# Performance work log

Measured on AMD Instinct MI355X. Metric: run time of the kernel, lower is better.

The kernel has to match this reference:

```python
import jax, jax.numpy as jnp
import numpy as np

DIM = 512
HEADS = 8
DIM_HEAD = 64
INNER = HEADS * DIM_HEAD  # 512
EPS = 1e-6


def setup_inputs() -> dict:
    key = jax.random.key(0)
    ks = jax.random.split(key, 6)
    B, N = 8, 2048
    x = jax.random.normal(ks[0], (B, N, DIM), dtype=jnp.float32)
    # nn.Linear stores weight as [out, in]; we keep that layout and transpose in matmul.
    w_qkv = jax.random.normal(ks[1], (3 * INNER, DIM), dtype=jnp.float32) * (1.0 / np.sqrt(DIM))
    w_proj = jax.random.normal(ks[2], (DIM, INNER), dtype=jnp.float32) * (1.0 / np.sqrt(INNER))
    b_proj = jax.random.normal(ks[3], (DIM,), dtype=jnp.float32) * 0.01
    ln_gamma = jnp.ones((DIM,), dtype=jnp.float32)
    ln_beta = jnp.zeros((DIM,), dtype=jnp.float32)
    return {"x": x, "w_qkv": w_qkv, "w_proj": w_proj, "b_proj": b_proj,
            "ln_gamma": ln_gamma, "ln_beta": ln_beta}


def reference(x, w_qkv, w_proj, b_proj, ln_gamma, ln_beta):
    B, N, D = x.shape
    H, Dh = HEADS, DIM_HEAD
    # LayerNorm (eps=1e-6)
    mu = jnp.mean(x, axis=-1, keepdims=True)
    var = jnp.mean(jnp.square(x - mu), axis=-1, keepdims=True)
    xn = (x - mu) * jax.lax.rsqrt(var + EPS) * ln_gamma + ln_beta
    # QKV projection (no bias)
    qkv = xn @ w_qkv.T  # [B, N, 3*INNER]
    q, k, v = jnp.split(qkv, 3, axis=-1)
    # [B, N, H, Dh] -> [B, H, N, Dh]
    q = q.reshape(B, N, H, Dh).transpose(0, 2, 1, 3)
    k = k.reshape(B, N, H, Dh).transpose(0, 2, 1, 3)
    v = v.reshape(B, N, H, Dh).transpose(0, 2, 1, 3)
    scale = Dh ** (-0.5)
    attn = jnp.einsum('bhnd,bhmd->bhnm', q, k) * scale  # [B, H, N, N]
    attn = jax.nn.softmax(attn, axis=-1)
    out = jnp.einsum('bhnm,bhmd->bhnd', attn, v)  # [B, H, N, Dh]
    out = out.transpose(0, 2, 1, 3).reshape(B, N, H * Dh)
    out = out @ w_proj.T + b_proj
    return out
```

## Files before the change

### kernel.cpp

```cpp
#include <hip/hip_runtime.h>

typedef unsigned short u16;
typedef __bf16 bf16x8 __attribute__((ext_vector_type(8)));
typedef float f32x4 __attribute__((ext_vector_type(4)));

#define DIMD 512
#define SEQN 2048
#define NB   8
#define NH   8
#define DH   64
#define BHN  (NB*NH)
#define MROWS (NB*SEQN)
#define QSCALE 0.18033688f

__device__ __forceinline__ u16 f2bf(float f) {
  union { float f; unsigned u; } x; x.f = f;
  unsigned r = x.u + 0x7fffu + ((x.u >> 16) & 1u);
  return (u16)(r >> 16);
}
__device__ __forceinline__ u16 f2bf_fast(float f) {
  union { float f; unsigned u; } x; x.f = f;
  return (u16)((x.u + 0x8000u) >> 16);
}

__device__ __forceinline__ void gll16(const u16* g, u16* lbase) {
#if __has_builtin(__builtin_amdgcn_global_load_lds)
  __builtin_amdgcn_global_load_lds(
      (const __attribute__((address_space(1))) unsigned int*)g,
      (__attribute__((address_space(3))) unsigned int*)lbase, 16, 0, 0);
#else
  *(uint4*)((u16*)lbase + (threadIdx.x & 63) * 8) = *(const uint4*)g;
#endif
}

__global__ __launch_bounds__(256) void wcvt2(
    const float* __restrict__ wa, const float* __restrict__ wb,
    u16* __restrict__ oa, u16* __restrict__ ob, int na, int nb) {
  int i = (blockIdx.x * 256 + threadIdx.x) * 8;
  const float* src; u16* dst; int idx;
  if (i < na) { src = wa; dst = oa; idx = i; }
  else { idx = i - na; if (idx >= nb) return; src = wb; dst = ob; }
  float4 f0 = *(const float4*)(src + idx);
  float4 f1 = *(const float4*)(src + idx + 4);
  union { uint4 v; u16 s[8]; } u;
  u.s[0] = f2bf(f0.x); u.s[1] = f2bf(f0.y); u.s[2] = f2bf(f0.z); u.s[3] = f2bf(f0.w);
  u.s[4] = f2bf(f1.x); u.s[5] = f2bf(f1.y); u.s[6] = f2bf(f1.z); u.s[7] = f2bf(f1.w);
  *(uint4*)(dst + idx) = u.v;
}

__global__ __launch_bounds__(256) void ln_kernel(
    const float* __restrict__ x, const float* __restrict__ gamma,
    const float* __restrict__ beta, u16* __restrict__ xn) {
  int row = blockIdx.x * 4 + (threadIdx.x >> 6);
  int lane = threadIdx.x & 63;
  const float* xr = x + (size_t)row * DIMD;
  float f[8], g[8], b[8];
  *(float4*)&f[0] = *(const float4*)(xr + lane * 8);
  *(float4*)&f[4] = *(const float4*)(xr + lane * 8 + 4);
  *(float4*)&g[0] = *(const float4*)(gamma + lane * 8);
  *(float4*)&g[4] = *(const float4*)(gamma + lane * 8 + 4);
  *(float4*)&b[0] = *(const float4*)(beta + lane * 8);
  *(float4*)&b[4] = *(const float4*)(beta + lane * 8 + 4);
  float sum = 0.f, sq = 0.f;
#pragma unroll
  for (int i = 0; i < 8; ++i) { sum += f[i]; sq += f[i] * f[i]; }
#pragma unroll
  for (int off = 1; off < 64; off <<= 1) {
    sum += __shfl_xor(sum, off, 64);
    sq  += __shfl_xor(sq, off, 64);
  }
  float mean = sum * (1.0f / DIMD);
  float var = sq * (1.0f / DIMD) - mean * mean;
  float rstd = rsqrtf(var + 1e-6f);
  union { uint4 v; u16 s[8]; } uo;
#pragma unroll
  for (int i = 0; i < 8; ++i)
    uo.s[i] = f2bf((f[i] - mean) * rstd * g[i] + b[i]);
  *(uint4*)(xn + (size_t)row * DIMD + lane * 8) = uo.v;
}

__global__ __launch_bounds__(256) void qkv_gemm(
    const u16* __restrict__ A, const u16* __restrict__ Bm,
    u16* __restrict__ qo, u16* __restrict__ ko, u16* __restrict__ vto) {
  __shared__ __align__(16) u16 la[128 * 64];
  __shared__ __align__(16) u16 lb[128 * 64];
  const int K = DIMD;
  int tid = threadIdx.x;
  int bm = blockIdx.x, bn = blockIdx.y;
  int wid = tid >> 6, lane = tid & 63, lm = lane & 15, quad = lane >> 4;
  int wm = wid >> 1, wn = wid & 1;
  int lsw = lm & 7;
  f32x4 acc[4][4] = {};
  const u16* Ab = A + (size_t)(bm * 128) * K;
  const u16* Bb = Bm + (size_t)(bn * 128) * K;
  int cb_row = lane >> 3, cb_sub = lane & 7;
  int xsrc = (cb_sub ^ cb_row) * 8;
  for (int k0 = 0; k0 < K; k0 += 64) {
    __syncthreads();
#pragma unroll
    for (int r = 0; r < 4; ++r) {
      int seg = wid * 4 + r;
      int row = seg * 8 + cb_row;
      size_t goff = (size_t)row * K + k0 + xsrc;
      gll16(Ab + goff, &la[seg * 512]);
      gll16(Bb + goff, &lb[seg * 512]);
    }
    __syncthreads();
#pragma unroll
    for (int h = 0; h < 2; ++h) {
      bf16x8 af[4], bfr[4];
#pragma unroll
      for (int i = 0; i < 4; ++i)
        af[i] = *(const bf16x8*)&la[(wm * 64 + i * 16 + lm) * 64 + (((h * 4 + quad) ^ lsw) * 8)];
#pragma unroll
      for (int j = 0; j < 4; ++j)
        bfr[j] = *(const bf16x8*)&lb[(wn * 64 + j * 16 + lm) * 64 + (((h * 4 + quad) ^ lsw) * 8)];
#pragma unroll
      for (int i = 0; i < 4; ++i)
#pragma unroll
        for (int j = 0; j < 4; ++j)
          acc[i][j] = __builtin_amdgcn_mfma_f32_16x16x32_bf16(af[i], bfr[j], acc[i][j], 0, 0, 0);
    }
  }
  int part = bn >> 2;
  if (part == 2) {
#pragma unroll
    for (int i = 0; i < 4; ++i)
#pragma unroll
      for (int j = 0; j < 4; ++j) {
        int col = bn * 128 + wn * 64 + j * 16 + lm;
        int rem = col & 511, h = rem >> 6, d = rem & 63;
        int rg = bm * 128 + wm * 64 + i * 16 + quad * 4;
        int b = rg >> 11, nn = rg & 2047;
        union { unsigned long long ll; u16 s4[4]; } pk;
#pragma unroll
        for (int r = 0; r < 4; ++r) pk.s4[r] = f2bf(acc[i][j][r]);
        *(unsigned long long*)&vto[((size_t)(b * NH + h) * DH + d) * SEQN + nn] = pk.ll;
      }
  } else {
    u16* dst = part ? ko : qo;
    float sc = part ? 1.0f : QSCALE;
#pragma unroll
    for (int i = 0; i < 4; ++i)
#pragma unroll
      for (int j = 0; j < 4; ++j) {
        int col = bn * 128 + wn * 64 + j * 16 + lm;
        int rem = col & 511, h = rem >> 6, d = rem & 63;
#pragma unroll
        for (int r = 0; r < 4; ++r) {
          int rg = bm * 128 + wm * 64 + i * 16 + quad * 4 + r;
          int b = rg >> 11, nn = rg & 2047;
          dst[((size_t)(b * NH + h) * SEQN + nn) * DH + d] = f2bf(acc[i][j][r] * sc);
        }
      }
  }
}

__global__ __launch_bounds__(512, 4) void attn_kernel(
    const u16* __restrict__ q, const u16* __restrict__ k,
    const u16* __restrict__ vt, u16* __restrict__ att) {
  __shared__ __align__(16) u16 kt[2][64 * 64];
  __shared__ __align__(16) u16 vtt[2][64 * 64];
  __shared__ __align__(16) u16 plds[8 * 16 * 64];
  int bh = blockIdx.x;
  int wid = threadIdx.x >> 6, lane = threadIdx.x & 63;
  int lm = lane & 15, quad = lane >> 4;
  int qrow0 = blockIdx.y * 256 + wid * 32;
  const u16* qb = q + (size_t)bh * SEQN * DH;
  const u16* kb = k + (size_t)bh * SEQN * DH;
  const u16* vb = vt + (size_t)bh * DH * SEQN;
  u16* pw = plds + wid * (16 * 64);

  int cb_row = lane >> 3, cb_sub = lane & 7;
  int xstage = (cb_sub ^ cb_row) * 8;
  int xsw = quad ^ (lm & 7);
  int lsw = lm & 7;

  bf16x8 ones;
#pragma unroll
  for (int i = 0; i < 8; ++i) ones[i] = (__bf16)1.0f;

  bf16x8 qf[2][2];
#pragma unroll
  for (int g = 0; g < 2; ++g)
#pragma unroll
    for (int c = 0; c < 2; ++c)
      qf[g][c] = *(const bf16x8*)(qb + (size_t)(qrow0 + g * 16 + lm) * DH + c * 32 + quad * 8);

  f32x4 Ot[2][4] = {};
  f32x4 lacc[2] = {};

  auto stage = [&](int bsel, int j0) {
    if (wid < 4) {
#pragma unroll
      for (int i = 0; i < 2; ++i) {
        int seg = wid * 2 + i;
        int row = seg * 8 + cb_row;
        gll16(kb + (size_t)(j0 + row) * DH + xstage, &kt[bsel][seg * 512]);
      }
    } else {
#pragma unroll
      for (int i = 0; i < 2; ++i) {
        int seg = (wid - 4) * 2 + i;
        int row = seg * 8 + cb_row;
        gll16(vb + (size_t)row * SEQN + j0 + xstage, &vtt[bsel][seg * 512]);
      }
    }
  };

  stage(0, 0);
  for (int t = 0; t < SEQN / 64; ++t) {
    int bsel = t & 1;
    __syncthreads();
    if (t + 1 < SEQN / 64) stage(bsel ^ 1, (t + 1) * 64);

    bf16x8 kf[4][2];
#pragma unroll
    for (int js = 0; js < 4; ++js) {
      int row = js * 16 + lm;
      kf[js][0] = *(const bf16x8*)&kt[bsel][row * 64 + xsw * 8];
      kf[js][1] = *(const bf16x8*)&kt[bsel][row * 64 + (xsw ^ 4) * 8];
    }
    bf16x8 pa[2][2];
#pragma unroll
    for (int g = 0; g < 2; ++g) {
#pragma unroll
      for (int js = 0; js < 4; ++js) {
        f32x4 z = {0.f, 0.f, 0.f, 0.f};
        z = __builtin_amdgcn_mfma_f32_16x16x32_bf16(kf[js][0], qf[g][0], z, 0, 0, 0);
        z = __builtin_amdgcn_mfma_f32_16x16x32_bf16(kf[js][1], qf[g][1], z, 0, 0, 0);
        union { unsigned long long ll; u16 s4[4]; } pk;
#pragma unroll
        for (int r = 0; r < 4; ++r)
          pk.s4[r] = f2bf_fast(__builtin_amdgcn_exp2f(z[r]));
        int wc = (js * 2 + (quad >> 1)) ^ lsw;
        *(unsigned long long*)&pw[lm * 64 + wc * 8 + (quad & 1) * 4] = pk.ll;
      }
      pa[g][0] = *(const bf16x8*)&pw[lm * 64 + (quad ^ lsw) * 8];
      pa[g][1] = *(const bf16x8*)&pw[lm * 64 + ((4 + quad) ^ lsw) * 8];
      lacc[g] = __builtin_amdgcn_mfma_f32_16x16x32_bf16(ones, pa[g][0], lacc[g], 0, 0, 0);
      lacc[g] = __builtin_amdgcn_mfma_f32_16x16x32_bf16(ones, pa[g][1], lacc[g], 0, 0, 0);
    }
#pragma unroll
    for (int db = 0; db < 4; ++db) {
      int row = db * 16 + lm;
      bf16x8 va0 = *(const bf16x8*)&vtt[bsel][row * 64 + xsw * 8];
      bf16x8 va1 = *(const bf16x8*)&vtt[bsel][row * 64 + (xsw ^ 4) * 8];
      Ot[0][db] = __builtin_amdgcn_mfma_f32_16x16x32_bf16(va0, pa[0][0], Ot[0][db], 0, 0, 0);
      Ot[0][db] = __builtin_amdgcn_mfma_f32_16x16x32_bf16(va1, pa[0][1], Ot[0][db], 0, 0, 0);
      Ot[1][db] = __builtin_amdgcn_mfma_f32_16x16x32_bf16(va0, pa[1][0], Ot[1][db], 0, 0, 0);
      Ot[1][db] = __builtin_amdgcn_mfma_f32_16x16x32_bf16(va1, pa[1][1], Ot[1][db], 0, 0, 0);
    }
  }
  int b = bh >> 3, h = bh & 7;
#pragma unroll
  for (int g = 0; g < 2; ++g) {
    float inv = 1.0f / lacc[g][0];
    size_t rowoff = ((size_t)(b * SEQN + qrow0 + g * 16 + lm)) * DIMD + h * DH;
#pragma unroll
    for (int db = 0; db < 4; ++db) {
      union { unsigned long long ll; u16 s4[4]; } ok;
#pragma unroll
      for (int r = 0; r < 4; ++r) ok.s4[r] = f2bf(Ot[g][db][r] * inv);
      *(unsigned long long*)&att[rowoff + db * 16 + quad * 4] = ok.ll;
    }
  }
}

__global__ __launch_bounds__(256) void proj_gemm(
    const u16* __restrict__ A, const u16* __restrict__ Bm,
    const float* __restrict__ bias, float* __restrict__ C) {
  __shared__ __align__(16) u16 la[128 * 64];
  __shared__ __align__(16) u16 lb[128 * 64];
  const int K = DIMD, N = DIMD;
  int tid = threadIdx.x;
  int bm = blockIdx.x, bn = blockIdx.y;
  int wid = tid >> 6, lane = tid & 63, lm = lane & 15, quad = lane >> 4;
  int wm = wid >> 1, wn = wid & 1;
  int lsw = lm & 7;
  f32x4 acc[4][4] = {};
  const u16* Ab = A + (size_t)(bm * 128) * K;
  const u16* Bb = Bm + (size_t)(bn * 128) * K;
  int cb_row = lane >> 3, cb_sub = lane & 7;
  int xsrc = (cb_sub ^ cb_row) * 8;
  for (int k0 = 0; k0 < K; k0 += 64) {
    __syncthreads();
#pragma unroll
    for (int r = 0; r < 4; ++r) {
      int seg = wid * 4 + r;
      int row = seg * 8 + cb_row;
      size_t goff = (size_t)row * K + k0 + xsrc;
      gll16(Ab + goff, &la[seg * 512]);
      gll16(Bb + goff, &lb[seg * 512]);
    }
    __syncthreads();
#pragma unroll
    for (int h = 0; h < 2; ++h) {
      bf16x8 af[4], bfr[4];
#pragma unroll
      for (int i = 0; i < 4; ++i)
        af[i] = *(const bf16x8*)&la[(wm * 64 + i * 16 + lm) * 64 + (((h * 4 + quad) ^ lsw) * 8)];
#pragma unroll
      for (int j = 0; j < 4; ++j)
        bfr[j] = *(const bf16x8*)&lb[(wn * 64 + j * 16 + lm) * 64 + (((h * 4 + quad) ^ lsw) * 8)];
#pragma unroll
      for (int i = 0; i < 4; ++i)
#pragma unroll
        for (int j = 0; j < 4; ++j)
          acc[i][j] = __builtin_amdgcn_mfma_f32_16x16x32_bf16(af[i], bfr[j], acc[i][j], 0, 0, 0);
    }
  }
#pragma unroll
  for (int i = 0; i < 4; ++i)
#pragma unroll
    for (int j = 0; j < 4; ++j) {
      int col = bn * 128 + wn * 64 + j * 16 + lm;
      float bv = bias[col];
#pragma unroll
      for (int r = 0; r < 4; ++r) {
        int rg = bm * 128 + wm * 64 + i * 16 + quad * 4 + r;
        C[(size_t)rg * N + col] = acc[i][j][r] + bv;
      }
    }
}

extern "C" void kernel_launch(void* const* d_in, const int* in_sizes, int n_in,
                              void* d_out, int out_size, void* d_ws, size_t ws_size,
                              hipStream_t stream) {
  const float* x      = (const float*)d_in[0];
  const float* w_qkv  = (const float*)d_in[1];
  const float* w_proj = (const float*)d_in[2];
  const float* b_proj = (const float*)d_in[3];
  const float* gamma  = (const float*)d_in[4];
  const float* beta   = (const float*)d_in[5];
  float* out = (float*)d_out;

  const size_t SZ = (size_t)MROWS * DIMD;
  u16* xn  = (u16*)d_ws;
  u16* q   = xn + SZ;
  u16* kk  = q + SZ;
  u16* vt  = kk + SZ;
  u16* wqb = vt + SZ;
  u16* wpb = wqb + (size_t)3 * DIMD * DIMD;
  u16* att = xn;

  const int NQKV = 3 * DIMD * DIMD;
  const int NPRJ = DIMD * DIMD;
  wcvt2<<<dim3((NQKV + NPRJ) / 2048), dim3(256), 0, stream>>>(
      w_qkv, w_proj, wqb, wpb, NQKV, NPRJ);
  ln_kernel<<<dim3(MROWS / 4), dim3(256), 0, stream>>>(x, gamma, beta, xn);
  qkv_gemm<<<dim3(MROWS / 128, (3 * DIMD) / 128), dim3(256), 0, stream>>>(
      xn, wqb, q, kk, vt);
  attn_kernel<<<dim3(BHN, SEQN / 256), dim3(512), 0, stream>>>(q, kk, vt, att);
  proj_gemm<<<dim3(MROWS / 128, DIMD / 128), dim3(256), 0, stream>>>(
      att, wpb, b_proj, out);
}
```

Measured before the change: 220.5 us.

## Swap MFMA operands for vectorized epilogue stores; add setprio and native bf16 converts

The Q/K and projection GEMMs now swap the MFMA A/B operands, so each lane holds four consecutive columns of one row. This lets the epilogues write 8-byte bf16 packs and float4 outputs with a vectorized bias load, replacing the earlier scattered scalar stores. The attention kernel wraps its MFMA groups in s_setprio, uses native __bf16 casts instead of manual bit rounding, and uses a hardware reciprocal for the final normalisation. The bf16 cast changes rounding in the exp path and rcp is approximate, so the numerics shift slightly.

Measured after the change: 217.8 us. No clear change (-1.2%).

```diff
diff --git a/kernel.cpp b/kernel.cpp
--- a/kernel.cpp
+++ b/kernel.cpp
@@ -17,10 +17,6 @@
   union { float f; unsigned u; } x; x.f = f;
   unsigned r = x.u + 0x7fffu + ((x.u >> 16) & 1u);
   return (u16)(r >> 16);
-}
-__device__ __forceinline__ u16 f2bf_fast(float f) {
-  union { float f; unsigned u; } x; x.f = f;
-  return (u16)((x.u + 0x8000u) >> 16);
 }
 
 __device__ __forceinline__ void gll16(const u16* g, u16* lbase) {
@@ -90,6 +86,7 @@
   int wid = tid >> 6, lane = tid & 63, lm = lane & 15, quad = lane >> 4;
   int wm = wid >> 1, wn = wid & 1;
   int lsw = lm & 7;
+  int part = bn >> 2;
   f32x4 acc[4][4] = {};
   const u16* Ab = A + (size_t)(bm * 128) * K;
   const u16* Bb = Bm + (size_t)(bn * 128) * K;
@@ -115,14 +112,21 @@
 #pragma unroll
       for (int j = 0; j < 4; ++j)
         bfr[j] = *(const bf16x8*)&lb[(wn * 64 + j * 16 + lm) * 64 + (((h * 4 + quad) ^ lsw) * 8)];
-#pragma unroll
-      for (int i = 0; i < 4; ++i)
-#pragma unroll
-        for (int j = 0; j < 4; ++j)
-          acc[i][j] = __builtin_amdgcn_mfma_f32_16x16x32_bf16(af[i], bfr[j], acc[i][j], 0, 0, 0);
-    }
-  }
-  int part = bn >> 2;
+      if (part == 2) {
+#pragma unroll
+        for (int i = 0; i < 4; ++i)
+#pragma unroll
+          for (int j = 0; j < 4; ++j)
+            acc[i][j] = __builtin_amdgcn_mfma_f32_16x16x32_bf16(af[i], bfr[j], acc[i][j], 0, 0, 0);
+      } else {
+#pragma unroll
+        for (int i = 0; i < 4; ++i)
+#pragma unroll
+          for (int j = 0; j < 4; ++j)
+            acc[i][j] = __builtin_amdgcn_mfma_f32_16x16x32_bf16(bfr[j], af[i], acc[i][j], 0, 0, 0);
+      }
+    }
+  }
   if (part == 2) {
 #pragma unroll
     for (int i = 0; i < 4; ++i)
@@ -144,14 +148,14 @@
     for (int i = 0; i < 4; ++i)
 #pragma unroll
       for (int j = 0; j < 4; ++j) {
-        int col = bn * 128 + wn * 64 + j * 16 + lm;
-        int rem = col & 511, h = rem >> 6, d = rem & 63;
-#pragma unroll
-        for (int r = 0; r < 4; ++r) {
-          int rg = bm * 128 + wm * 64 + i * 16 + quad * 4 + r;
-          int b = rg >> 11, nn = rg & 2047;
-          dst[((size_t)(b * NH + h) * SEQN + nn) * DH + d] = f2bf(acc[i][j][r] * sc);
-        }
+        int rg = bm * 128 + wm * 64 + i * 16 + lm;
+        int b = rg >> 11, nn = rg & 2047;
+        int col = bn * 128 + wn * 64 + j * 16 + quad * 4;
+        int rem = col & 511, hh = rem >> 6, d = rem & 63;
+        union { unsigned long long ll; __bf16 h4[4]; } pk;
+#pragma unroll
+        for (int r = 0; r < 4; ++r) pk.h4[r] = (__bf16)(acc[i][j][r] * sc);
+        *(unsigned long long*)&dst[((size_t)(b * NH + hh) * SEQN + nn) * DH + d] = pk.ll;
       }
   }
 }
@@ -227,41 +231,47 @@
 #pragma unroll
       for (int js = 0; js < 4; ++js) {
         f32x4 z = {0.f, 0.f, 0.f, 0.f};
+        __builtin_amdgcn_s_setprio(1);
         z = __builtin_amdgcn_mfma_f32_16x16x32_bf16(kf[js][0], qf[g][0], z, 0, 0, 0);
         z = __builtin_amdgcn_mfma_f32_16x16x32_bf16(kf[js][1], qf[g][1], z, 0, 0, 0);
-        union { unsigned long long ll; u16 s4[4]; } pk;
+        __builtin_amdgcn_s_setprio(0);
+        union { unsigned long long ll; __bf16 h4[4]; } pk;
 #pragma unroll
         for (int r = 0; r < 4; ++r)
-          pk.s4[r] = f2bf_fast(__builtin_amdgcn_exp2f(z[r]));
+          pk.h4[r] = (__bf16)__builtin_amdgcn_exp2f(z[r]);
         int wc = (js * 2 + (quad >> 1)) ^ lsw;
         *(unsigned long long*)&pw[lm * 64 + wc * 8 + (quad & 1) * 4] = pk.ll;
       }
       pa[g][0] = *(const bf16x8*)&pw[lm * 64 + (quad ^ lsw) * 8];
       pa[g][1] = *(const bf16x8*)&pw[lm * 64 + ((4 + quad) ^ lsw) * 8];
+      __builtin_amdgcn_s_setprio(1);
       lacc[g] = __builtin_amdgcn_mfma_f32_16x16x32_bf16(ones, pa[g][0], lacc[g], 0, 0, 0);
       lacc[g] = __builtin_amdgcn_mfma_f32_16x16x32_bf16(ones, pa[g][1], lacc[g], 0, 0, 0);
+      __builtin_amdgcn_s_setprio(0);
     }
 #pragma unroll
     for (int db = 0; db < 4; ++db) {
       int row = db * 16 + lm;
       bf16x8 va0 = *(const bf16x8*)&vtt[bsel][row * 64 + xsw * 8];
       bf16x8 va1 = *(const bf16x8*)&vtt[bsel][row * 64 + (xsw ^ 4) * 8];
+      __builtin_amdgcn_s_setprio(1);
       Ot[0][db] = __builtin_amdgcn_mfma_f32_16x16x32_bf16(va0, pa[0][0], Ot[0][db], 0, 0, 0);
       Ot[0][db] = __builtin_amdgcn_mfma_f32_16x16x32_bf16(va1, pa[0][1], Ot[0][db], 0, 0, 0);
       Ot[1][db] = __builtin_amdgcn_mfma_f32_16x16x32_bf16(va0, pa[1][0], Ot[1][db], 0, 0, 0);
       Ot[1][db] = __builtin_amdgcn_mfma_f32_16x16x32_bf16(va1, pa[1][1], Ot[1][db], 0, 0, 0);
+      __builtin_amdgcn_s_setprio(0);
     }
   }
   int b = bh >> 3, h = bh & 7;
 #pragma unroll
   for (int g = 0; g < 2; ++g) {
-    float inv = 1.0f / lacc[g][0];
+    float inv = __builtin_amdgcn_rcpf(lacc[g][0]);
     size_t rowoff = ((size_t)(b * SEQN + qrow0 + g * 16 + lm)) * DIMD + h * DH;
 #pragma unroll
     for (int db = 0; db < 4; ++db) {
-      union { unsigned long long ll; u16 s4[4]; } ok;
-#pragma unroll
-      for (int r = 0; r < 4; ++r) ok.s4[r] = f2bf(Ot[g][db][r] * inv);
+      union { unsigned long long ll; __bf16 h4[4]; } ok;
+#pragma unroll
+      for (int r = 0; r < 4; ++r) ok.h4[r] = (__bf16)(Ot[g][db][r] * inv);
       *(unsigned long long*)&att[rowoff + db * 16 + quad * 4] = ok.ll;
     }
   }
@@ -307,20 +317,20 @@
       for (int i = 0; i < 4; ++i)
 #pragma unroll
         for (int j = 0; j < 4; ++j)
-          acc[i][j] = __builtin_amdgcn_mfma_f32_16x16x32_bf16(af[i], bfr[j], acc[i][j], 0, 0, 0);
+          acc[i][j] = __builtin_amdgcn_mfma_f32_16x16x32_bf16(bfr[j], af[i], acc[i][j], 0, 0, 0);
     }
   }
 #pragma unroll
   for (int i = 0; i < 4; ++i)
 #pragma unroll
     for (int j = 0; j < 4; ++j) {
-      int col = bn * 128 + wn * 64 + j * 16 + lm;
-      float bv = bias[col];
-#pragma unroll
-      for (int r = 0; r < 4; ++r) {
-        int rg = bm * 128 + wm * 64 + i * 16 + quad * 4 + r;
-        C[(size_t)rg * N + col] = acc[i][j][r] + bv;
-      }
+      int rg = bm * 128 + wm * 64 + i * 16 + lm;
+      int col = bn * 128 + wn * 64 + j * 16 + quad * 4;
+      float4 bv = *(const float4*)(bias + col);
+      float4 o;
+      o.x = acc[i][j][0] + bv.x; o.y = acc[i][j][1] + bv.y;
+      o.z = acc[i][j][2] + bv.z; o.w = acc[i][j][3] + bv.w;
+      *(float4*)&C[(size_t)rg * N + col] = o;
     }
 }
 
```
